# Kernel optimization log

Measured on AMD Instinct MI355X. Metric: run time of the kernel, lower is better.

Reference implementation:

```python
import jax, jax.numpy as jnp
import numpy as np
import math

MODEL_DIM = 1024
HEAD_DIM = 64
NUM_HEADS = 16
FF_MULT = 4
FF_DIM = FF_MULT * MODEL_DIM
ATTN_DIM = NUM_HEADS * HEAD_DIM
FUSED_DIMS = (ATTN_DIM, ATTN_DIM, ATTN_DIM, FF_DIM, FF_DIM)


def setup_inputs() -> dict:
    key = jax.random.key(0)
    k_x, k_in, k_attn, k_ff = jax.random.split(key, 4)
    B, S = 2, 2048
    inputs = jax.random.normal(k_x, (B, S, MODEL_DIM), dtype=jnp.float32)
    # LayerNorm affine params (torch defaults: weight=1, bias=0)
    ln_w = jnp.ones((MODEL_DIM,), dtype=jnp.float32)
    ln_b = jnp.zeros((MODEL_DIM,), dtype=jnp.float32)
    # Linear weights stored as [in, out] (equivalent to torch W.T)
    s_in = 1.0 / math.sqrt(MODEL_DIM)
    w_in = jax.random.uniform(k_in, (MODEL_DIM, sum(FUSED_DIMS)), jnp.float32, -s_in, s_in)
    s_a = 1.0 / math.sqrt(ATTN_DIM)
    w_attn = jax.random.uniform(k_attn, (ATTN_DIM, MODEL_DIM), jnp.float32, -s_a, s_a)
    s_f = 1.0 / math.sqrt(FF_DIM)
    w_ff = jax.random.uniform(k_ff, (FF_DIM, MODEL_DIM), jnp.float32, -s_f, s_f)
    return {"inputs": inputs, "ln_w": ln_w, "ln_b": ln_b,
            "w_in": w_in, "w_attn": w_attn, "w_ff": w_ff}


def _layer_norm(x, w, b, eps=1e-5):
    mu = jnp.mean(x, axis=-1, keepdims=True)
    var = jnp.var(x, axis=-1, keepdims=True)
    return (x - mu) * jax.lax.rsqrt(var + eps) * w + b


def reference(inputs, ln_w, ln_b, w_in, w_attn, w_ff):
    B, S, D = inputs.shape
    units = _layer_norm(inputs, ln_w, ln_b)
    proj = units @ w_in                                   # [B,S,3*A+2*F]
    splits = np.cumsum(FUSED_DIMS)[:-1]
    q, k, v, ff, ff_gate = jnp.split(proj, splits, axis=-1)
    # split heads: [B,S,H*d] -> [B,H,S,d]
    def heads(t):
        return t.reshape(B, S, NUM_HEADS, HEAD_DIM).transpose(0, 2, 1, 3)
    q, k, v = heads(q), heads(k), heads(v)
    scale = 1.0 / math.sqrt(HEAD_DIM)
    score = jnp.einsum('bhsd,bhTd->bhsT', q, k) * scale   # [B,H,S,S]
    weight = jax.nn.softmax(score, axis=-1)
    attn = jnp.einsum('bhsT,bhTd->bhsd', weight, v)       # [B,H,S,d]
    concat = attn.transpose(0, 2, 1, 3).reshape(B, S, ATTN_DIM)
    attn_out = concat @ w_attn                            # [B,S,D]
    ff_out = (ff * jax.nn.gelu(ff_gate, approximate=True)) @ w_ff
    return inputs + attn_out + ff_out
```

## Files before the change

kernel.cpp:

```cpp
#include <hip/hip_runtime.h>
#include <hip/hip_bf16.h>
#include <cstdint>
#include <cstddef>

typedef __bf16 bf16;
typedef __bf16 bf16x8 __attribute__((ext_vector_type(8)));
typedef float f32x4 __attribute__((ext_vector_type(4)));

#define MFMA16(a, b, c) __builtin_amdgcn_mfma_f32_16x16x32_bf16(a, b, c, 0, 0, 0)

#define GLOBAL_LOAD_LDS16(gptr, lptr)                                          \
  __builtin_amdgcn_global_load_lds(                                            \
      (const __attribute__((address_space(1))) void*)(gptr),                   \
      (__attribute__((address_space(3))) void*)(lptr), 16, 0, 0)

__global__ __launch_bounds__(256) void prep(const float* __restrict__ w_in,
                                            const float* __restrict__ w_attn,
                                            const float* __restrict__ w_ff,
                                            bf16* __restrict__ wt_in,
                                            bf16* __restrict__ wtcat,
                                            const float* __restrict__ x,
                                            const float* __restrict__ ln_w,
                                            const float* __restrict__ ln_b,
                                            bf16* __restrict__ xn) {
  __shared__ __align__(16) char sm[4352];
  if (blockIdx.x < 16384) {
    float(*t)[33] = (float(*)[33])sm;
    int id = blockIdx.x;
    const float* src; bf16* dst;
    int srcN, srccol0, LDO, mode, obase, goff, kcol0, ntn;
    if (id < 3072) {
      src = w_in; dst = wt_in; srcN = 11264; srccol0 = 0; LDO = 1024;
      mode = 0; obase = 0; goff = 0; kcol0 = 0; ntn = 96;
    } else if (id < 7168) {
      id -= 3072; src = w_in; dst = wt_in; srcN = 11264; srccol0 = 3072;
      LDO = 1024; mode = 1; obase = 3072; goff = 0; kcol0 = 0; ntn = 128;
    } else if (id < 11264) {
      id -= 7168; src = w_in; dst = wt_in; srcN = 11264; srccol0 = 7168;
      LDO = 1024; mode = 1; obase = 3072; goff = 64; kcol0 = 0; ntn = 128;
    } else if (id < 12288) {
      id -= 11264; src = w_attn; dst = wtcat; srcN = 1024; srccol0 = 0;
      LDO = 5120; mode = 0; obase = 0; goff = 0; kcol0 = 0; ntn = 32;
    } else {
      id -= 12288; src = w_ff; dst = wtcat; srcN = 1024; srccol0 = 0;
      LDO = 5120; mode = 0; obase = 0; goff = 0; kcol0 = 1024; ntn = 32;
    }
    const int n0 = (id % ntn) * 32, k0 = (id / ntn) * 32;
    const int tx = threadIdx.x & 31, ty = threadIdx.x >> 5;
    for (int i = ty; i < 32; i += 8)
      t[i][tx] = src[(size_t)(k0 + i) * srcN + srccol0 + n0 + tx];
    __syncthreads();
    for (int i = ty; i < 32; i += 8) {
      int n = n0 + i;
      int orow = mode ? (obase + ((n >> 6) << 7) + goff + (n & 63)) : (obase + n);
      dst[(size_t)orow * LDO + kcol0 + k0 + tx] = (bf16)t[tx][i];
    }
  } else {
    float* rs = (float*)sm;
    float* rss = rs + 256;
    const int row = blockIdx.x - 16384;
    const int tid = threadIdx.x;
    const float* xr = x + (size_t)row * 1024;
    float4 v = *(const float4*)&xr[tid * 4];
    float s = v.x + v.y + v.z + v.w;
    float ss = v.x * v.x + v.y * v.y + v.z * v.z + v.w * v.w;
    rs[tid] = s; rss[tid] = ss;
    __syncthreads();
    for (int off = 128; off > 0; off >>= 1) {
      if (tid < off) { rs[tid] += rs[tid + off]; rss[tid] += rss[tid + off]; }
      __syncthreads();
    }
    const float mean = rs[0] * (1.f / 1024.f);
    const float var = rss[0] * (1.f / 1024.f) - mean * mean;
    const float rstd = rsqrtf(var + 1e-5f);
    const float* vp = (const float*)&v;
    for (int i = 0; i < 4; i++) {
      int c = tid * 4 + i;
      xn[(size_t)row * 1024 + c] = (bf16)((vp[i] - mean) * rstd * ln_w[c] + ln_b[c]);
    }
  }
}

__global__ __launch_bounds__(256) void vtrans(const bf16* __restrict__ proj,
                                              bf16* __restrict__ vt) {
  __shared__ bf16 t[64][80];
  const int tid = threadIdx.x;
  const int s0 = blockIdx.x * 64;
  const int h = blockIdx.y, b = blockIdx.z;
  constexpr size_t LDP = 3072;
  const bf16* src = proj + (size_t)b * 2048 * LDP + 2048 + h * 64;
  {
    int s = tid >> 2, d0 = (tid & 3) * 16;
    *(bf16x8*)&t[s][d0]     = *(const bf16x8*)&src[(size_t)(s0 + s) * LDP + d0];
    *(bf16x8*)&t[s][d0 + 8] = *(const bf16x8*)&src[(size_t)(s0 + s) * LDP + d0 + 8];
  }
  __syncthreads();
  {
    int d = tid >> 2, sb = (tid & 3) * 16;
    bf16* dst = vt + ((size_t)(b * 16 + h) * 64 + d) * 2048 + s0 + sb;
    bf16x8 o0, o1;
    for (int i = 0; i < 8; i++) { o0[i] = t[sb + i][d]; o1[i] = t[sb + 8 + i][d]; }
    *(bf16x8*)&dst[0] = o0;
    *(bf16x8*)&dst[8] = o1;
  }
}

__global__ __launch_bounds__(256) void flash_attn(const bf16* __restrict__ proj,
                                                  const bf16* __restrict__ vt,
                                                  bf16* __restrict__ hcat) {
  __shared__ __align__(16) char smem[50176];
  bf16* Ks = (bf16*)smem;
  bf16* Vs = (bf16*)(smem + 16384);
  bf16* Ps = (bf16*)(smem + 32768);
  const int tid = threadIdx.x;
  const int wave = tid >> 6, lane = tid & 63;
  const int quad = lane >> 4, l16 = lane & 15;
  const int q0 = blockIdx.x * 64;
  const int h = blockIdx.y, b = blockIdx.z;
  constexpr size_t LDP = 3072;
  const bf16* Qb = proj + (size_t)b * 2048 * LDP + h * 64;
  const bf16* Kb = proj + (size_t)b * 2048 * LDP + 1024 + h * 64;
  const bf16* Vt = vt + (size_t)(b * 16 + h) * 64 * 2048;

  const int qrow = q0 + wave * 16 + l16;
  bf16x8 aq0r = *(const bf16x8*)&Qb[(size_t)qrow * LDP + quad * 8];
  bf16x8 aq1r = *(const bf16x8*)&Qb[(size_t)qrow * LDP + 32 + quad * 8];
  bf16x8 aq0, aq1;
#pragma unroll
  for (int i = 0; i < 8; i++) {
    aq0[i] = (bf16)((float)aq0r[i] * 0.125f);
    aq1[i] = (bf16)((float)aq1r[i] * 0.125f);
  }

  f32x4 O[4] = {};
  float plrow[4] = {0.f, 0.f, 0.f, 0.f};

  const int krow_ = wave * 8 + (lane >> 3);
  const int kq_ = ((lane & 7) ^ (krow_ & 7)) * 8;
  const int vrow_ = wave * 4 + (lane >> 4);
  const int vq_ = ((lane & 15) ^ (vrow_ & 15)) * 8;

  for (int j0 = 0; j0 < 2048; j0 += 128) {
#pragma unroll
    for (int p = 0; p < 4; p++) {
      int kr = p * 32 + krow_;
      GLOBAL_LOAD_LDS16(&Kb[(size_t)(j0 + kr) * LDP + kq_],
                        &Ks[kr * 64 + (lane & 7) * 8]);
      int vr = p * 16 + vrow_;
      GLOBAL_LOAD_LDS16(&Vt[(size_t)vr * 2048 + j0 + vq_],
                        &Vs[vr * 128 + (lane & 15) * 8]);
    }
    __syncthreads();

    f32x4 sa[8];
#pragma unroll
    for (int nt = 0; nt < 8; nt++) {
      int r = nt * 16 + l16;
      bf16x8 bk0 = *(const bf16x8*)&Ks[r * 64 + (quad ^ (r & 7)) * 8];
      bf16x8 bk1 = *(const bf16x8*)&Ks[r * 64 + ((quad + 4) ^ (r & 7)) * 8];
      f32x4 t = {};
      t = MFMA16(aq0, bk0, t);
      sa[nt] = MFMA16(aq1, bk1, t);
    }

    bf16* Pw = Ps + wave * (16 * 136);
#pragma unroll
    for (int r = 0; r < 4; r++) {
      bf16* pr = &Pw[(quad * 4 + r) * 136];
      float ts = 0.f;
#pragma unroll
      for (int nt = 0; nt < 8; nt++) {
        float p = __expf(sa[nt][r]);
        pr[nt * 16 + l16] = (bf16)p;
        ts += p;
      }
      plrow[r] += ts;
    }

#pragma unroll
    for (int kg = 0; kg < 4; kg++) {
      bf16x8 aP = *(const bf16x8*)&Pw[l16 * 136 + kg * 32 + quad * 8];
#pragma unroll
      for (int nb = 0; nb < 4; nb++) {
        int vrr = nb * 16 + l16;
        int vsl = ((kg * 4 + quad) ^ (vrr & 15)) * 8;
        bf16x8 bv = *(const bf16x8*)&Vs[vrr * 128 + vsl];
        O[nb] = MFMA16(aP, bv, O[nb]);
      }
    }
    __syncthreads();
  }

#pragma unroll
  for (int r = 0; r < 4; r++) {
    float ts = plrow[r];
#pragma unroll
    for (int d = 1; d < 16; d <<= 1) ts += __shfl_xor(ts, d, 64);
    float inv = 1.f / ts;
    size_t row = (size_t)b * 2048 + q0 + wave * 16 + quad * 4 + r;
#pragma unroll
    for (int nb = 0; nb < 4; nb++)
      hcat[row * 5120 + h * 64 + nb * 16 + l16] = (bf16)(O[nb][r] * inv);
  }
}

__global__ __launch_bounds__(256) void gemm_proj(const bf16* __restrict__ A,
                                                 const bf16* __restrict__ Bt,
                                                 bf16* __restrict__ proj,
                                                 bf16* __restrict__ hcat) {
  constexpr int K = 1024, LDC = 136;
  __shared__ __align__(16) char smem[17408];
  bf16* As = (bf16*)smem;
  bf16* Bs = As + 128 * 32;
  bf16* Cs = (bf16*)smem;
  const int tid = threadIdx.x;
  const int wave = tid >> 6, lane = tid & 63;
  const int quad = lane >> 4, l16 = lane & 15;
  constexpr int NM = 4, NN = 4;
  const int wm0 = (wave >> 1) * 64, wn0 = (wave & 1) * 64;
  const size_t rowA0 = (size_t)blockIdx.y * 128;
  const size_t rowB0 = (size_t)blockIdx.x * 128;

  const int srow = wave * 16 + (lane >> 2);
  const int sq = ((lane & 3) ^ ((lane >> 3) & 3)) * 8;
  const int sslot = (lane & 3) * 8;
  const int rslot = (quad ^ ((l16 >> 1) & 3)) * 8;

  f32x4 acc[NM][NN] = {};

  for (int k0 = 0; k0 < K; k0 += 32) {
#pragma unroll
    for (int p = 0; p < 2; p++) {
      int r = p * 64 + srow;
      GLOBAL_LOAD_LDS16(&A[(rowA0 + r) * K + k0 + sq], &As[r * 32 + sslot]);
      GLOBAL_LOAD_LDS16(&Bt[(rowB0 + r) * K + k0 + sq], &Bs[r * 32 + sslot]);
    }
    __syncthreads();
    bf16x8 af[NM], bfr[NN];
#pragma unroll
    for (int i = 0; i < NM; i++)
      af[i] = *(const bf16x8*)&As[(wm0 + i * 16 + l16) * 32 + rslot];
#pragma unroll
    for (int j = 0; j < NN; j++)
      bfr[j] = *(const bf16x8*)&Bs[(wn0 + j * 16 + l16) * 32 + rslot];
#pragma unroll
    for (int i = 0; i < NM; i++)
#pragma unroll
      for (int j = 0; j < NN; j++)
        acc[i][j] = MFMA16(af[i], bfr[j], acc[i][j]);
    __syncthreads();
  }

#pragma unroll
  for (int half = 0; half < 2; half++) {
    if ((wave >> 1) == half) {
#pragma unroll
      for (int i = 0; i < NM; i++)
#pragma unroll
        for (int j = 0; j < NN; j++)
#pragma unroll
          for (int r = 0; r < 4; r++)
            Cs[(i * 16 + quad * 4 + r) * LDC + wn0 + j * 16 + l16] =
                (bf16)acc[i][j][r];
    }
    __syncthreads();
    if (blockIdx.x < 24) {
      const int c0 = (tid & 15) * 8;
#pragma unroll
      for (int it = 0; it < 4; it++) {
        int row = (tid >> 4) + it * 16;
        *(bf16x8*)&proj[(rowA0 + half * 64 + row) * 3072 + rowB0 + c0] =
            *(const bf16x8*)&Cs[row * LDC + c0];
      }
    } else {
      const int T = blockIdx.x - 24;
      const int c0 = (tid & 7) * 8;
#pragma unroll
      for (int p = 0; p < 2; p++) {
        int row = (tid >> 3) + p * 32;
        bf16x8 f = *(const bf16x8*)&Cs[row * LDC + c0];
        bf16x8 g = *(const bf16x8*)&Cs[row * LDC + 64 + c0];
        bf16x8 o;
#pragma unroll
        for (int i = 0; i < 8; i++) {
          float xg = (float)g[i];
          float u = 0.7978845608f * (xg + 0.044715f * xg * xg * xg);
          float gl = xg / (1.f + __expf(-2.f * u));
          o[i] = (bf16)((float)f[i] * gl);
        }
        *(bf16x8*)&hcat[(rowA0 + half * 64 + row) * 5120 + 1024 + T * 64 + c0] = o;
      }
    }
    __syncthreads();
  }
}

__global__ __launch_bounds__(256) void gemm_out(const bf16* __restrict__ A,
                                                const bf16* __restrict__ Bt,
                                                bf16* __restrict__ part) {
  constexpr int LDAB = 5120, LDC = 136;
  __shared__ __align__(16) char smem[32768];
  bf16* As = (bf16*)smem;
  bf16* Bs = As + 128 * 64;
  bf16* Cs = (bf16*)smem;
  const int tid = threadIdx.x;
  const int wave = tid >> 6, lane = tid & 63;
  const int quad = lane >> 4, l16 = lane & 15;
  constexpr int NM = 4, NN = 4;
  const int wm0 = (wave >> 1) * 64, wn0 = (wave & 1) * 64;
  const size_t rowA0 = (size_t)blockIdx.y * 128;
  const size_t rowB0 = (size_t)blockIdx.x * 128;
  const int kbeg = blockIdx.z * 1280, kend = kbeg + 1280;

  const int srow = tid >> 3;
  const int sq = ((tid & 7) ^ (srow & 7)) * 8;
  const int sslot = (tid & 7) * 8;

  f32x4 acc[NM][NN] = {};

  for (int k0 = kbeg; k0 < kend; k0 += 64) {
#pragma unroll
    for (int p = 0; p < 4; p++) {
      int r = p * 32 + srow;
      GLOBAL_LOAD_LDS16(&A[(rowA0 + r) * LDAB + k0 + sq], &As[r * 64 + sslot]);
      GLOBAL_LOAD_LDS16(&Bt[(rowB0 + r) * LDAB + k0 + sq], &Bs[r * 64 + sslot]);
    }
    __syncthreads();
#pragma unroll
    for (int c = 0; c < 2; c++) {
      bf16x8 af[NM], bfr[NN];
#pragma unroll
      for (int i = 0; i < NM; i++) {
        int r = wm0 + i * 16 + l16;
        af[i] = *(const bf16x8*)&As[r * 64 + ((c * 4 + quad) ^ (r & 7)) * 8];
      }
#pragma unroll
      for (int j = 0; j < NN; j++) {
        int r = wn0 + j * 16 + l16;
        bfr[j] = *(const bf16x8*)&Bs[r * 64 + ((c * 4 + quad) ^ (r & 7)) * 8];
      }
#pragma unroll
      for (int i = 0; i < NM; i++)
#pragma unroll
        for (int j = 0; j < NN; j++)
          acc[i][j] = MFMA16(af[i], bfr[j], acc[i][j]);
    }
    __syncthreads();
  }

  bf16* dst = part + (size_t)blockIdx.z * (4096 * 1024);
#pragma unroll
  for (int half = 0; half < 2; half++) {
    if ((wave >> 1) == half) {
#pragma unroll
      for (int i = 0; i < NM; i++)
#pragma unroll
        for (int j = 0; j < NN; j++)
#pragma unroll
          for (int r = 0; r < 4; r++)
            Cs[(i * 16 + quad * 4 + r) * LDC + wn0 + j * 16 + l16] =
                (bf16)acc[i][j][r];
    }
    __syncthreads();
    const int c0 = (tid & 15) * 8;
#pragma unroll
    for (int it = 0; it < 4; it++) {
      int row = (tid >> 4) + it * 16;
      *(bf16x8*)&dst[(rowA0 + half * 64 + row) * 1024 + rowB0 + c0] =
          *(const bf16x8*)&Cs[row * LDC + c0];
    }
    __syncthreads();
  }
}

__global__ __launch_bounds__(256) void reduce_out(const float* __restrict__ x,
                                                  const bf16* __restrict__ part,
                                                  float* __restrict__ out) {
  const size_t i = ((size_t)blockIdx.x * 256 + threadIdx.x) * 8;
  constexpr size_t SL = 4096 * 1024;
  float r[8];
  float4 x0 = *(const float4*)&x[i];
  float4 x1 = *(const float4*)&x[i + 4];
  r[0] = x0.x; r[1] = x0.y; r[2] = x0.z; r[3] = x0.w;
  r[4] = x1.x; r[5] = x1.y; r[6] = x1.z; r[7] = x1.w;
#pragma unroll
  for (int z = 0; z < 4; z++) {
    bf16x8 p = *(const bf16x8*)&part[z * SL + i];
#pragma unroll
    for (int k = 0; k < 8; k++) r[k] += (float)p[k];
  }
  float4 o0 = {r[0], r[1], r[2], r[3]};
  float4 o1 = {r[4], r[5], r[6], r[7]};
  *(float4*)&out[i] = o0;
  *(float4*)&out[i + 4] = o1;
}

extern "C" void kernel_launch(void* const* d_in, const int* in_sizes, int n_in,
                              void* d_out, int out_size, void* d_ws, size_t ws_size,
                              hipStream_t stream) {
  const float* x      = (const float*)d_in[0];
  const float* ln_w   = (const float*)d_in[1];
  const float* ln_b   = (const float*)d_in[2];
  const float* w_in   = (const float*)d_in[3];
  const float* w_attn = (const float*)d_in[4];
  const float* w_ff   = (const float*)d_in[5];
  float* out = (float*)d_out;
  char* ws = (char*)d_ws;

  bf16* wt_in = (bf16*)(ws);
  bf16* wtcat = (bf16*)(ws + 23068672);
  bf16* xn    = (bf16*)(ws + 33554432);
  bf16* proj  = (bf16*)(ws + 41943040);
  bf16* part  = (bf16*)(ws + 67108864);
  bf16* vt    = (bf16*)(ws + 100663296);
  bf16* hcat  = (bf16*)(ws + 134217728);

  prep<<<20480, 256, 0, stream>>>(w_in, w_attn, w_ff, wt_in, wtcat,
                                  x, ln_w, ln_b, xn);
  gemm_proj<<<dim3(88, 32), 256, 0, stream>>>(xn, wt_in, proj, hcat);
  vtrans<<<dim3(32, 16, 2), 256, 0, stream>>>(proj, vt);
  flash_attn<<<dim3(32, 16, 2), 256, 0, stream>>>(proj, vt, hcat);
  gemm_out<<<dim3(8, 32, 4), 256, 0, stream>>>(hcat, wtcat, part);
  reduce_out<<<2048, 256, 0, stream>>>(x, part, out);
}
```

Before: 403.0 us.

## Enlarge gemm_proj tile to 256x256 with triple-buffered async LDS pipeline

Rewrites the input-projection GEMM to use 256x256 output tiles with 512 threads (8 waves, each 128x64), and a 3-stage LDS ring of global_load_lds copies. Each k-step is gated by vmcnt waits and a single barrier, replacing the previous two syncthreads per step. It also raises MFMA wave priority during compute. The aim is to overlap global loads with MFMA work and improve operand reuse per byte loaded. In exchange it uses 96KB of LDS and more accumulator registers per thread, which cuts occupancy, and launches fewer blocks (704 versus 2816).

```diff
diff --git a/kernel.cpp b/kernel.cpp
--- a/kernel.cpp
+++ b/kernel.cpp
@@ -204,94 +204,128 @@
   }
 }
 
-__global__ __launch_bounds__(256) void gemm_proj(const bf16* __restrict__ A,
-                                                 const bf16* __restrict__ Bt,
-                                                 bf16* __restrict__ proj,
-                                                 bf16* __restrict__ hcat) {
-  constexpr int K = 1024, LDC = 136;
-  __shared__ __align__(16) char smem[17408];
-  bf16* As = (bf16*)smem;
-  bf16* Bs = As + 128 * 32;
-  bf16* Cs = (bf16*)smem;
+__global__ __launch_bounds__(512, 2) void gemm_proj(const bf16* __restrict__ A,
+                                                    const bf16* __restrict__ Bt,
+                                                    bf16* __restrict__ proj,
+                                                    bf16* __restrict__ hcat) {
+  constexpr int K = 1024, NT = 32;
+  __shared__ __align__(16) char smem[98304];
   const int tid = threadIdx.x;
   const int wave = tid >> 6, lane = tid & 63;
   const int quad = lane >> 4, l16 = lane & 15;
-  constexpr int NM = 4, NN = 4;
-  const int wm0 = (wave >> 1) * 64, wn0 = (wave & 1) * 64;
-  const size_t rowA0 = (size_t)blockIdx.y * 128;
-  const size_t rowB0 = (size_t)blockIdx.x * 128;
-
-  const int srow = wave * 16 + (lane >> 2);
-  const int sq = ((lane & 3) ^ ((lane >> 3) & 3)) * 8;
-  const int sslot = (lane & 3) * 8;
+  const int wm0 = (wave >> 2) * 128, wn0 = (wave & 3) * 64;
+  const size_t rowA0 = (size_t)blockIdx.y * 256;
+  const size_t rowB0 = (size_t)blockIdx.x * 256;
+  const bf16* Ag = A + rowA0 * K;
+  const bf16* Bg = Bt + rowB0 * K;
+
+  const int srow = tid >> 2;
+  const int sslot = tid & 3;
   const int rslot = (quad ^ ((l16 >> 1) & 3)) * 8;
 
-  f32x4 acc[NM][NN] = {};
-
-  for (int k0 = 0; k0 < K; k0 += 32) {
+  f32x4 acc[8][4] = {};
+
+  auto STAGE = [&](int kt, int buf) {
+    bf16* As = (bf16*)(smem + buf * 32768);
+    bf16* Bs = As + 256 * 32;
+    const int k0 = kt * 32;
 #pragma unroll
     for (int p = 0; p < 2; p++) {
-      int r = p * 64 + srow;
-      GLOBAL_LOAD_LDS16(&A[(rowA0 + r) * K + k0 + sq], &As[r * 32 + sslot]);
-      GLOBAL_LOAD_LDS16(&Bt[(rowB0 + r) * K + k0 + sq], &Bs[r * 32 + sslot]);
-    }
-    __syncthreads();
-    bf16x8 af[NM], bfr[NN];
-#pragma unroll
-    for (int i = 0; i < NM; i++)
-      af[i] = *(const bf16x8*)&As[(wm0 + i * 16 + l16) * 32 + rslot];
-#pragma unroll
-    for (int j = 0; j < NN; j++)
+      int r = p * 128 + srow;
+      int kq = (sslot ^ ((r >> 1) & 3)) * 8;
+      GLOBAL_LOAD_LDS16(&Ag[(size_t)r * K + k0 + kq], &As[r * 32 + sslot * 8]);
+      GLOBAL_LOAD_LDS16(&Bg[(size_t)r * K + k0 + kq], &Bs[r * 32 + sslot * 8]);
+    }
+  };
+
+  STAGE(0, 0);
+  STAGE(1, 1);
+  asm volatile("s_waitcnt vmcnt(4)" ::: "memory");
+  __builtin_amdgcn_s_barrier();
+  asm volatile("" ::: "memory");
+
+  int cbuf = 0, sbuf = 2;
+#pragma unroll 1
+  for (int kt = 0; kt < NT; kt++) {
+    if (kt + 2 < NT) STAGE(kt + 2, sbuf);
+    const bf16* As = (const bf16*)(smem + cbuf * 32768);
+    const bf16* Bs = As + 256 * 32;
+    bf16x8 bfr[4];
+#pragma unroll
+    for (int j = 0; j < 4; j++)
       bfr[j] = *(const bf16x8*)&Bs[(wn0 + j * 16 + l16) * 32 + rslot];
 #pragma unroll
-    for (int i = 0; i < NM; i++)
-#pragma unroll
-      for (int j = 0; j < NN; j++)
-        acc[i][j] = MFMA16(af[i], bfr[j], acc[i][j]);
-    __syncthreads();
-  }
-
-#pragma unroll
-  for (int half = 0; half < 2; half++) {
-    if ((wave >> 1) == half) {
-#pragma unroll
-      for (int i = 0; i < NM; i++)
-#pragma unroll
-        for (int j = 0; j < NN; j++)
-#pragma unroll
-          for (int r = 0; r < 4; r++)
-            Cs[(i * 16 + quad * 4 + r) * LDC + wn0 + j * 16 + l16] =
-                (bf16)acc[i][j][r];
-    }
-    __syncthreads();
-    if (blockIdx.x < 24) {
-      const int c0 = (tid & 15) * 8;
-#pragma unroll
-      for (int it = 0; it < 4; it++) {
-        int row = (tid >> 4) + it * 16;
-        *(bf16x8*)&proj[(rowA0 + half * 64 + row) * 3072 + rowB0 + c0] =
-            *(const bf16x8*)&Cs[row * LDC + c0];
-      }
+    for (int ih = 0; ih < 2; ih++) {
+      bf16x8 af[4];
+#pragma unroll
+      for (int i = 0; i < 4; i++)
+        af[i] = *(const bf16x8*)&As[(wm0 + (ih * 4 + i) * 16 + l16) * 32 + rslot];
+      __builtin_amdgcn_s_setprio(1);
+#pragma unroll
+      for (int i = 0; i < 4; i++)
+#pragma unroll
+        for (int j = 0; j < 4; j++)
+          acc[ih * 4 + i][j] = MFMA16(af[i], bfr[j], acc[ih * 4 + i][j]);
+      __builtin_amdgcn_s_setprio(0);
+    }
+    if (kt + 2 < NT) {
+      asm volatile("s_waitcnt vmcnt(4)" ::: "memory");
     } else {
-      const int T = blockIdx.x - 24;
-      const int c0 = (tid & 7) * 8;
-#pragma unroll
-      for (int p = 0; p < 2; p++) {
-        int row = (tid >> 3) + p * 32;
-        bf16x8 f = *(const bf16x8*)&Cs[row * LDC + c0];
-        bf16x8 g = *(const bf16x8*)&Cs[row * LDC + 64 + c0];
-        bf16x8 o;
-#pragma unroll
-        for (int i = 0; i < 8; i++) {
-          float xg = (float)g[i];
-          float u = 0.7978845608f * (xg + 0.044715f * xg * xg * xg);
-          float gl = xg / (1.f + __expf(-2.f * u));
-          o[i] = (bf16)((float)f[i] * gl);
+      asm volatile("s_waitcnt vmcnt(0)" ::: "memory");
+    }
+    __builtin_amdgcn_s_barrier();
+    asm volatile("" ::: "memory");
+    cbuf = (cbuf == 2) ? 0 : cbuf + 1;
+    sbuf = (sbuf == 2) ? 0 : sbuf + 1;
+  }
+
+  {
+    const int T2 = (int)blockIdx.x - 12;
+    bf16* Cs = (bf16*)smem;
+    constexpr int LDC2 = 264;
+#pragma unroll 1
+    for (int h = 0; h < 2; h++) {
+      if ((wave >> 2) == h) {
+#pragma unroll
+        for (int i = 0; i < 8; i++)
+#pragma unroll
+          for (int j = 0; j < 4; j++)
+#pragma unroll
+            for (int r = 0; r < 4; r++)
+              Cs[(i * 16 + quad * 4 + r) * LDC2 + wn0 + j * 16 + l16] =
+                  (bf16)acc[i][j][r];
+      }
+      __syncthreads();
+      if (T2 < 0) {
+#pragma unroll
+        for (int it = 0; it < 8; it++) {
+          int idx = it * 512 + tid;
+          int row = idx >> 5, ch = (idx & 31) * 8;
+          *(bf16x8*)&proj[(rowA0 + h * 128 + row) * 3072 + rowB0 + ch] =
+              *(const bf16x8*)&Cs[row * LDC2 + ch];
         }
-        *(bf16x8*)&hcat[(rowA0 + half * 64 + row) * 5120 + 1024 + T * 64 + c0] = o;
-      }
-    }
-    __syncthreads();
+      } else {
+#pragma unroll
+        for (int it = 0; it < 4; it++) {
+          int idx = it * 512 + tid;
+          int row = idx >> 4;
+          int p = (idx >> 3) & 1, c8 = (idx & 7) * 8;
+          bf16x8 f = *(const bf16x8*)&Cs[row * LDC2 + p * 128 + c8];
+          bf16x8 g = *(const bf16x8*)&Cs[row * LDC2 + p * 128 + 64 + c8];
+          bf16x8 o;
+#pragma unroll
+          for (int i = 0; i < 8; i++) {
+            float xg = (float)g[i];
+            float u = 0.7978845608f * (xg + 0.044715f * xg * xg * xg);
+            float gl = xg / (1.f + __expf(-2.f * u));
+            o[i] = (bf16)((float)f[i] * gl);
+          }
+          *(bf16x8*)&hcat[(rowA0 + h * 128 + row) * 5120 + 1024 +
+                          (2 * T2 + p) * 64 + c8] = o;
+        }
+      }
+      __syncthreads();
+    }
   }
 }
 
@@ -417,7 +451,7 @@
 
   prep<<<20480, 256, 0, stream>>>(w_in, w_attn, w_ff, wt_in, wtcat,
                                   x, ln_w, ln_b, xn);
-  gemm_proj<<<dim3(88, 32), 256, 0, stream>>>(xn, wt_in, proj, hcat);
+  gemm_proj<<<dim3(44, 16), 512, 0, stream>>>(xn, wt_in, proj, hcat);
   vtrans<<<dim3(32, 16, 2), 256, 0, stream>>>(proj, vt);
   flash_attn<<<dim3(32, 16, 2), 256, 0, stream>>>(proj, vt, hcat);
   gemm_out<<<dim3(8, 32, 4), 256, 0, stream>>>(hcat, wtcat, part);
```

Result: faster. 392.1 us (-2.7%).
